# Optimization experiments

Hardware: AMD Instinct MI355X
Metric: run time of the kernel (lower is better)

Reference implementation:

```python
import jax, jax.numpy as jnp
import numpy as np

N, F_IN, H, E, G = 100000, 128, 64, 1600000, 256
BN_EPS = 1e-5


def setup_inputs() -> dict:
    key = jax.random.key(0)
    ks = jax.random.split(key, 32)
    rn = lambda k, shp, s=0.1: jax.random.normal(k, shp, jnp.float32) * s
    ru = lambda k, shp: jax.random.uniform(k, shp, jnp.float32)
    inp = {
        'x': jax.random.normal(ks[0], (N, F_IN), jnp.float32),
        'edge_index': jax.random.randint(ks[1], (2, E), 0, N),
        'batch': jnp.sort(jax.random.randint(ks[2], (N,), 0, G)),
        'w0': rn(ks[3], (F_IN, H)), 'b0': rn(ks[4], (H,)),
        'w1': rn(ks[5], (H, H)), 'b1': rn(ks[6], (H,)),
        'w2': rn(ks[7], (H, H)), 'b2': rn(ks[8], (H,)),
        'g0': ru(ks[9], (H,)) + 0.5, 'beta0': rn(ks[10], (H,)),
        'm0': rn(ks[11], (H,)), 'v0': ru(ks[12], (H,)) + 0.5,
        'g1': ru(ks[13], (H,)) + 0.5, 'beta1': rn(ks[14], (H,)),
        'm1': rn(ks[15], (H,)), 'v1': ru(ks[16], (H,)) + 0.5,
        'g2': ru(ks[17], (H,)) + 0.5, 'beta2': rn(ks[18], (H,)),
        'm2': rn(ks[19], (H,)), 'v2': ru(ks[20], (H,)) + 0.5,
        'l1w': rn(ks[21], (H, H // 2)), 'l1b': rn(ks[22], (H // 2,)),
        'l2w': rn(ks[23], (H // 2, 2)), 'l2b': rn(ks[24], (2,)),
    }
    return inp


def reference(x, edge_index, batch, w0, b0, w1, b1, w2, b2,
              g0, beta0, m0, v0, g1, beta1, m1, v1, g2, beta2, m2, v2,
              l1w, l1b, l2w, l2b):
    n = x.shape[0]
    # GCN: add self-loops, symmetric normalization deg^{-1/2} A_hat deg^{-1/2}
    loop = jnp.arange(n)
    src = jnp.concatenate([edge_index[0], loop])
    dst = jnp.concatenate([edge_index[1], loop])
    deg = jax.ops.segment_sum(jnp.ones_like(src, dtype=x.dtype), dst, num_segments=n)
    dinv = jax.lax.rsqrt(jnp.maximum(deg, 1.0))  # deg >= 1 after self-loops
    norm = (dinv[src] * dinv[dst])[:, None]      # [E+N, 1]

    def gcn(h, w, b):
        h = h @ w                                              # [N, H]
        agg = jax.ops.segment_sum(h[src] * norm, dst, num_segments=n)
        return agg + b

    def bn(h, g, be, m, v):  # eval-mode BatchNorm1d (running stats)
        return (h - m) * (g * jax.lax.rsqrt(v + BN_EPS)) + be

    h = jax.nn.relu(bn(gcn(x, w0, b0), g0, beta0, m0, v0))
    h = jax.nn.relu(bn(gcn(h, w1, b1), g1, beta1, m1, v1))
    h = jax.nn.relu(bn(gcn(h, w2, b2), g2, beta2, m2, v2))
    pooled = jax.ops.segment_sum(h, batch, num_segments=G)     # global_add_pool
    h = jax.nn.relu(pooled @ l1w + l1b)
    return h @ l2w + l2b                                        # [G, 2]
```

## Files before the change

### kernel.cpp

```cpp
#include <hip/hip_runtime.h>
#include <hip/hip_bf16.h>

#define BN_EPS 1e-5f

typedef short bf16x8 __attribute__((ext_vector_type(8)));
typedef float f32x4 __attribute__((ext_vector_type(4)));

static __device__ __forceinline__ unsigned short f2bf(float f) {
    unsigned u = __float_as_uint(f);
    unsigned r = (u + 0x7FFF + ((u >> 16) & 1)) >> 16;
    return (unsigned short)r;
}
static __device__ __forceinline__ float bf2f(unsigned short s) {
    return __uint_as_float((unsigned)s << 16);
}
__device__ __forceinline__ int pad8i(int c) { return (c + 7) & ~7; }

#define BIN_SHIFT 9
#define BIN_NODES 512
#define P1_CHUNK 8192
#define IMG_CAP 12288
#define SCAN_CHUNK 1024

__global__ void scan_block_sums(const int* __restrict__ cnt, int* __restrict__ bsums, int n) {
    __shared__ int sdata[256];
    int b = blockIdx.x, t = threadIdx.x;
    int base = b * SCAN_CHUNK;
    int s = 0;
    for (int i = t; i < SCAN_CHUNK; i += 256) {
        int idx = base + i;
        if (idx < n) s += pad8i(cnt[idx]);
    }
    sdata[t] = s;
    __syncthreads();
    for (int off = 128; off > 0; off >>= 1) {
        if (t < off) sdata[t] += sdata[t + off];
        __syncthreads();
    }
    if (t == 0) bsums[b] = sdata[0];
}

__global__ void scan_block_exclusive(const int* __restrict__ in, int* __restrict__ out, int m) {
    __shared__ int sd[256];
    int t = threadIdx.x;
    int base = t * 4;
    int v0 = (base + 0 < m) ? in[base + 0] : 0;
    int v1 = (base + 1 < m) ? in[base + 1] : 0;
    int v2 = (base + 2 < m) ? in[base + 2] : 0;
    int v3 = (base + 3 < m) ? in[base + 3] : 0;
    int tsum = v0 + v1 + v2 + v3;
    sd[t] = tsum;
    __syncthreads();
    for (int off = 1; off < 256; off <<= 1) {
        int x = (t >= off) ? sd[t - off] : 0;
        __syncthreads();
        sd[t] += x;
        __syncthreads();
    }
    int excl = sd[t] - tsum;
    if (base + 0 < m) out[base + 0] = excl;
    if (base + 1 < m) out[base + 1] = excl + v0;
    if (base + 2 < m) out[base + 2] = excl + v0 + v1;
    if (base + 3 < m) out[base + 3] = excl + v0 + v1 + v2;
    if (t == 255) out[m] = sd[255];
}

__global__ void scan_write(const int* __restrict__ cnt, const int* __restrict__ bsums,
                           int* __restrict__ row_start, int n) {
    __shared__ int sdata[256];
    int b = blockIdx.x, t = threadIdx.x;
    int base = b * SCAN_CHUNK + t * 4;
    int v0 = 0, v1 = 0, v2 = 0, v3 = 0;
    if (base + 0 < n) v0 = pad8i(cnt[base + 0]);
    if (base + 1 < n) v1 = pad8i(cnt[base + 1]);
    if (base + 2 < n) v2 = pad8i(cnt[base + 2]);
    if (base + 3 < n) v3 = pad8i(cnt[base + 3]);
    int tsum = v0 + v1 + v2 + v3;
    sdata[t] = tsum;
    __syncthreads();
    for (int off = 1; off < 256; off <<= 1) {
        int x = (t >= off) ? sdata[t - off] : 0;
        __syncthreads();
        sdata[t] += x;
        __syncthreads();
    }
    int excl = sdata[t] - tsum + bsums[b];
    if (base + 0 < n) row_start[base + 0] = excl;
    if (base + 1 < n) row_start[base + 1] = excl + v0;
    if (base + 2 < n) row_start[base + 2] = excl + v0 + v1;
    if (base + 3 < n) row_start[base + 3] = excl + v0 + v1 + v2;
    if (n - 1 >= base && n - 1 < base + 4)
        row_start[n] = excl + v0 + v1 + v2 + v3;
}

__global__ __launch_bounds__(256) void binhist_kernel(const int* __restrict__ dst,
                                                      int* __restrict__ bincnt,
                                                      int e, int nbins) {
    __shared__ int hist[256];
    int t = threadIdx.x;
    hist[t] = 0;
    __syncthreads();
    int c0 = blockIdx.x * P1_CHUNK;
    int iend = c0 + P1_CHUNK; if (iend > e) iend = e;
    for (int i = c0 + t; i < iend; i += 256)
        atomicAdd(&hist[dst[i] >> BIN_SHIFT], 1);
    __syncthreads();
    if (t < nbins && hist[t] > 0) atomicAdd(&bincnt[t], hist[t]);
}

__global__ __launch_bounds__(256) void phase1_kernel(
        const int* __restrict__ src, const int* __restrict__ dst,
        const int* __restrict__ bstart_e, int* __restrict__ bincur,
        int* __restrict__ ebuf, int e, int nbins) {
    __shared__ int hist[256], base[256], cur[256];
    int t = threadIdx.x;
    int c0 = blockIdx.x * P1_CHUNK;
    int iend = c0 + P1_CHUNK; if (iend > e) iend = e;
    hist[t] = 0;
    __syncthreads();
    for (int i = c0 + t; i < iend; i += 256)
        atomicAdd(&hist[dst[i] >> BIN_SHIFT], 1);
    __syncthreads();
    if (t < nbins && hist[t] > 0)
        base[t] = bstart_e[t] + atomicAdd(&bincur[t], hist[t]);
    cur[t] = 0;
    __syncthreads();
    for (int i = c0 + t; i < iend; i += 256) {
        int s = src[i], d = dst[i];
        int b = d >> BIN_SHIFT;
        int r = atomicAdd(&cur[b], 1);
        ebuf[base[b] + r] = s | ((d & (BIN_NODES - 1)) << 17);
    }
}

__global__ __launch_bounds__(256) void bincount_kernel(
        const int* __restrict__ ebuf, const int* __restrict__ bstart_e,
        int* __restrict__ cnt, float* __restrict__ dinv,
        unsigned short* __restrict__ ha_sent, int n) {
    __shared__ int c512[BIN_NODES];
    int b = blockIdx.x, t = threadIdx.x;
    if (b == 0 && t < 64) ha_sent[t] = 0;
    for (int k = t; k < BIN_NODES; k += 256) c512[k] = 0;
    __syncthreads();
    int e0 = bstart_e[b], e1 = bstart_e[b + 1];
    for (int j = e0 + t; j < e1; j += 256)
        atomicAdd(&c512[ebuf[j] >> 17], 1);
    __syncthreads();
    int n0 = b * BIN_NODES;
    for (int k = t; k < BIN_NODES; k += 256) {
        int i = n0 + k;
        if (i < n) {
            int c = c512[k];
            cnt[i] = c;
            dinv[i] = rsqrtf((float)(c + 1));
        }
    }
}

__global__ __launch_bounds__(256) void phase2_kernel(
        const int* __restrict__ ebuf, const int* __restrict__ bstart_e,
        const int* __restrict__ row_start, int* __restrict__ csr,
        int* __restrict__ gcursor, int n, int sentinel) {
    __shared__ int image[IMG_CAP];
    __shared__ int lcur[BIN_NODES];
    int b = blockIdx.x, t = threadIdx.x;
    int n0 = b * BIN_NODES;
    int n1 = n0 + BIN_NODES; if (n1 > n) n1 = n;
    int rbase = row_start[n0];
    int rspan = row_start[n1] - rbase;
    int e0 = bstart_e[b], e1 = bstart_e[b + 1];
    for (int k = t; k < BIN_NODES; k += 256) lcur[k] = 0;
    if (rspan <= IMG_CAP) {
        for (int k = t; k < rspan; k += 256) image[k] = sentinel;
        __syncthreads();
        for (int j = e0 + t; j < e1; j += 256) {
            int en = ebuf[j];
            int s = en & 0x1FFFF;
            int dl = en >> 17;
            int pos = row_start[n0 + dl] - rbase + atomicAdd(&lcur[dl], 1);
            image[pos] = s;
        }
        __syncthreads();
        for (int k = t; k < rspan; k += 256) csr[rbase + k] = image[k];
    } else {
        for (int k = n0 + t; k < n1; k += 256) gcursor[k] = 0;
        __syncthreads();
        for (int j = e0 + t; j < e1; j += 256) {
            int en = ebuf[j];
            int s = en & 0x1FFFF;
            int dl = en >> 17;
            int pos = row_start[n0 + dl] + atomicAdd(&gcursor[n0 + dl], 1);
            csr[pos] = s;
        }
        __syncthreads();
        for (int k = t; k < n1 - n0; k += 256) {
            int node = n0 + k;
            int c = gcursor[node];
            for (int pos = row_start[node] + c; pos < row_start[node + 1]; pos++)
                csr[pos] = sentinel;
        }
    }
}

template<int K, bool BF16IN>
__global__ __launch_bounds__(256) void lin_mfma(const void* __restrict__ in_,
                                                const float* __restrict__ w,
                                                const float* __restrict__ dinv,
                                                unsigned short* __restrict__ outbf, int n) {
    constexpr int XS = K + 8;
    __shared__ unsigned short xs[64 * XS];
    __shared__ unsigned short wt[64 * XS];
    int t = threadIdx.x;
    int row0 = blockIdx.x * 64;
    int nrows = n - row0; if (nrows > 64) nrows = 64;

    {
        const float4* w4 = (const float4*)w;
        for (int idx = t; idx < K * 16; idx += 256) {
            int k = idx >> 4, c4 = (idx & 15) * 4;
            float4 v = w4[idx];
            wt[(c4 + 0) * XS + k] = f2bf(v.x);
            wt[(c4 + 1) * XS + k] = f2bf(v.y);
            wt[(c4 + 2) * XS + k] = f2bf(v.z);
            wt[(c4 + 3) * XS + k] = f2bf(v.w);
        }
    }
    if constexpr (BF16IN) {
        const uint4* in4 = (const uint4*)((const unsigned short*)in_ + (size_t)row0 * K);
        int total8 = nrows * (K / 8);
        for (int idx = t; idx < total8; idx += 256) {
            int r = idx / (K / 8), kk = idx - r * (K / 8);
            uint4 v = in4[idx];
            *(uint4*)&xs[r * XS + kk * 8] = v;
        }
    } else {
        const float4* in4 = (const float4*)((const float*)in_ + (size_t)row0 * K);
        int total4 = nrows * (K / 4);
        for (int idx = t; idx < total4; idx += 256) {
            int r = idx / (K / 4), kk = idx - r * (K / 4);
            float4 v = in4[idx];
            ushort4 s4;
            s4.x = f2bf(v.x); s4.y = f2bf(v.y); s4.z = f2bf(v.z); s4.w = f2bf(v.w);
            *(ushort4*)&xs[r * XS + kk * 4] = s4;
        }
    }
    __syncthreads();

    int lane = t & 63;
    int wid = t >> 6;
    int quad = lane >> 4;
    int l15 = lane & 15;

    f32x4 acc[4];
#pragma unroll
    for (int cg_ = 0; cg_ < 4; cg_++) acc[cg_] = (f32x4){0.f, 0.f, 0.f, 0.f};

    const unsigned short* xrow = &xs[(wid * 16 + l15) * XS + quad * 8];
#pragma unroll
    for (int kc = 0; kc < K / 32; kc++) {
        bf16x8 bfrag = *(const bf16x8*)(xrow + kc * 32);
#pragma unroll
        for (int cg_ = 0; cg_ < 4; cg_++) {
            bf16x8 afrag = *(const bf16x8*)&wt[(cg_ * 16 + l15) * XS + kc * 32 + quad * 8];
            acc[cg_] = __builtin_amdgcn_mfma_f32_16x16x32_bf16(afrag, bfrag, acc[cg_], 0, 0, 0);
        }
    }

    int grow = row0 + wid * 16 + l15;
    if (grow < n) {
        float dv = dinv[grow];
#pragma unroll
        for (int cg_ = 0; cg_ < 4; cg_++) {
            ushort4 st;
            st.x = f2bf(acc[cg_][0] * dv);
            st.y = f2bf(acc[cg_][1] * dv);
            st.z = f2bf(acc[cg_][2] * dv);
            st.w = f2bf(acc[cg_][3] * dv);
            *(ushort4*)&outbf[(size_t)grow * 64 + cg_ * 16 + quad * 4] = st;
        }
    }
}

__global__ __launch_bounds__(256) void agg_kernel(
        const unsigned short* __restrict__ hs, const int* __restrict__ row_start,
        const int* __restrict__ csr, const float* __restrict__ dinv,
        const float* __restrict__ bias, const float* __restrict__ gam,
        const float* __restrict__ bet, const float* __restrict__ mu,
        const float* __restrict__ var,
        unsigned short* __restrict__ out, int n) {
    int iw = blockIdx.x * 4 + (threadIdx.x >> 6);
    unsigned lane = threadIdx.x & 63;
    if (iw >= n) return;
    int i = __builtin_amdgcn_readfirstlane(iw);
    float acc = bf2f(hs[((unsigned)i << 6) + lane]);
    int rs = __builtin_amdgcn_readfirstlane(row_start[i]);
    int re = __builtin_amdgcn_readfirstlane(row_start[i + 1]);
    int j = rs;
    for (; j + 16 <= re; j += 16) {
        int s0 = __builtin_amdgcn_readfirstlane(csr[j + 0]);
        int s1 = __builtin_amdgcn_readfirstlane(csr[j + 1]);
        int s2 = __builtin_amdgcn_readfirstlane(csr[j + 2]);
        int s3 = __builtin_amdgcn_readfirstlane(csr[j + 3]);
        int s4 = __builtin_amdgcn_readfirstlane(csr[j + 4]);
        int s5 = __builtin_amdgcn_readfirstlane(csr[j + 5]);
        int s6 = __builtin_amdgcn_readfirstlane(csr[j + 6]);
        int s7 = __builtin_amdgcn_readfirstlane(csr[j + 7]);
        int s8 = __builtin_amdgcn_readfirstlane(csr[j + 8]);
        int s9 = __builtin_amdgcn_readfirstlane(csr[j + 9]);
        int sA = __builtin_amdgcn_readfirstlane(csr[j + 10]);
        int sB = __builtin_amdgcn_readfirstlane(csr[j + 11]);
        int sC = __builtin_amdgcn_readfirstlane(csr[j + 12]);
        int sD = __builtin_amdgcn_readfirstlane(csr[j + 13]);
        int sE = __builtin_amdgcn_readfirstlane(csr[j + 14]);
        int sF = __builtin_amdgcn_readfirstlane(csr[j + 15]);
        float h0 = bf2f(hs[((unsigned)s0 << 6) + lane]);
        float h1 = bf2f(hs[((unsigned)s1 << 6) + lane]);
        float h2 = bf2f(hs[((unsigned)s2 << 6) + lane]);
        float h3 = bf2f(hs[((unsigned)s3 << 6) + lane]);
        float h4 = bf2f(hs[((unsigned)s4 << 6) + lane]);
        float h5 = bf2f(hs[((unsigned)s5 << 6) + lane]);
        float h6 = bf2f(hs[((unsigned)s6 << 6) + lane]);
        float h7 = bf2f(hs[((unsigned)s7 << 6) + lane]);
        float h8 = bf2f(hs[((unsigned)s8 << 6) + lane]);
        float h9 = bf2f(hs[((unsigned)s9 << 6) + lane]);
        float hA = bf2f(hs[((unsigned)sA << 6) + lane]);
        float hB = bf2f(hs[((unsigned)sB << 6) + lane]);
        float hC = bf2f(hs[((unsigned)sC << 6) + lane]);
        float hD = bf2f(hs[((unsigned)sD << 6) + lane]);
        float hE = bf2f(hs[((unsigned)sE << 6) + lane]);
        float hF = bf2f(hs[((unsigned)sF << 6) + lane]);
        acc += (((h0 + h1) + (h2 + h3)) + ((h4 + h5) + (h6 + h7)))
             + (((h8 + h9) + (hA + hB)) + ((hC + hD) + (hE + hF)));
    }
    for (; j < re; j += 8) {
        int s0 = __builtin_amdgcn_readfirstlane(csr[j + 0]);
        int s1 = __builtin_amdgcn_readfirstlane(csr[j + 1]);
        int s2 = __builtin_amdgcn_readfirstlane(csr[j + 2]);
        int s3 = __builtin_amdgcn_readfirstlane(csr[j + 3]);
        int s4 = __builtin_amdgcn_readfirstlane(csr[j + 4]);
        int s5 = __builtin_amdgcn_readfirstlane(csr[j + 5]);
        int s6 = __builtin_amdgcn_readfirstlane(csr[j + 6]);
        int s7 = __builtin_amdgcn_readfirstlane(csr[j + 7]);
        float h0 = bf2f(hs[((unsigned)s0 << 6) + lane]);
        float h1 = bf2f(hs[((unsigned)s1 << 6) + lane]);
        float h2 = bf2f(hs[((unsigned)s2 << 6) + lane]);
        float h3 = bf2f(hs[((unsigned)s3 << 6) + lane]);
        float h4 = bf2f(hs[((unsigned)s4 << 6) + lane]);
        float h5 = bf2f(hs[((unsigned)s5 << 6) + lane]);
        float h6 = bf2f(hs[((unsigned)s6 << 6) + lane]);
        float h7 = bf2f(hs[((unsigned)s7 << 6) + lane]);
        acc += ((h0 + h1) + (h2 + h3)) + ((h4 + h5) + (h6 + h7));
    }
    float agg = acc * dinv[i];
    float scale = gam[lane] * rsqrtf(var[lane] + BN_EPS);
    float r = (agg + bias[lane] - mu[lane]) * scale + bet[lane];
    out[((unsigned)i << 6) + lane] = f2bf(r > 0.f ? r : 0.f);
}

#define POOL_CHUNK 64
__global__ __launch_bounds__(256) void pool_kernel(const unsigned short* __restrict__ h,
                                                   const int* __restrict__ batch,
                                                   float* __restrict__ pooled, int n) {
    int wid = blockIdx.x * 4 + (threadIdx.x >> 6);
    int lane = threadIdx.x & 63;
    int start = wid * POOL_CHUNK;
    if (start >= n) return;
    int end = start + POOL_CHUNK; if (end > n) end = n;
    int cur = batch[start];
    float acc = 0.f;
    for (int i = start; i < end; i++) {
        int b = batch[i];
        if (b != cur) {
            atomicAdd(&pooled[(size_t)cur * 64 + lane], acc);
            acc = 0.f; cur = b;
        }
        acc += bf2f(h[(size_t)i * 64 + lane]);
    }
    atomicAdd(&pooled[(size_t)cur * 64 + lane], acc);
}

__global__ void mlp_kernel(const float* __restrict__ pooled,
                           const float* __restrict__ l1w, const float* __restrict__ l1b,
                           const float* __restrict__ l2w, const float* __restrict__ l2b,
                           float* __restrict__ out) {
    int g = blockIdx.x;
    int lane = threadIdx.x;
    __shared__ float p[64];
    __shared__ float h1[32];
    p[lane] = pooled[(size_t)g * 64 + lane];
    __syncthreads();
    if (lane < 32) {
        float a = l1b[lane];
#pragma unroll 8
        for (int k = 0; k < 64; k++) a += p[k] * l1w[k * 32 + lane];
        h1[lane] = a > 0.f ? a : 0.f;
    }
    __syncthreads();
    if (lane < 2) {
        float a = l2b[lane];
#pragma unroll 8
        for (int j = 0; j < 32; j++) a += h1[j] * l2w[j * 2 + lane];
        out[g * 2 + lane] = a;
    }
}

extern "C" void kernel_launch(void* const* d_in, const int* in_sizes, int n_in,
                              void* d_out, int out_size, void* d_ws, size_t ws_size,
                              hipStream_t stream) {
    const float* x     = (const float*)d_in[0];
    const int*   ei    = (const int*)d_in[1];
    const int*   batch = (const int*)d_in[2];
    const float* w0 = (const float*)d_in[3];
    const float* b0 = (const float*)d_in[4];
    const float* w1 = (const float*)d_in[5];
    const float* b1 = (const float*)d_in[6];
    const float* w2 = (const float*)d_in[7];
    const float* b2 = (const float*)d_in[8];
    const float* g0 = (const float*)d_in[9];
    const float* be0 = (const float*)d_in[10];
    const float* m0 = (const float*)d_in[11];
    const float* v0 = (const float*)d_in[12];
    const float* g1 = (const float*)d_in[13];
    const float* be1 = (const float*)d_in[14];
    const float* m1 = (const float*)d_in[15];
    const float* v1 = (const float*)d_in[16];
    const float* g2 = (const float*)d_in[17];
    const float* be2 = (const float*)d_in[18];
    const float* m2 = (const float*)d_in[19];
    const float* v2 = (const float*)d_in[20];
    const float* l1w = (const float*)d_in[21];
    const float* l1b = (const float*)d_in[22];
    const float* l2w = (const float*)d_in[23];
    const float* l2b = (const float*)d_in[24];
    float* out = (float*)d_out;

    const int N = in_sizes[2];
    const int E = in_sizes[1] / 2;
    const int G = out_size / 2;
    const int NBINS = (N + BIN_NODES - 1) / BIN_NODES;
    const int NB = (N + SCAN_CHUNK - 1) / SCAN_CHUNK;

    const int* src = ei;
    const int* dst = ei + E;

    char* p = (char*)d_ws;
    auto alloc = [&](size_t bytes) -> void* {
        void* r = (void*)p;
        p += (bytes + 255) & ~(size_t)255;
        return r;
    };
    const size_t CSR_CAP = ((size_t)E + 8 * (size_t)N + 3) & ~(size_t)3;
    float* dinvp    = (float*)alloc((size_t)N * 4);
    int*   cnt      = (int*)alloc((size_t)N * 4);
    int*   row_start= (int*)alloc((size_t)(N + 1) * 4);
    int*   cursor   = (int*)alloc((size_t)N * 4);
    int*   bsums    = (int*)alloc((size_t)(NB + 1) * 4);
    int*   bincnt   = (int*)alloc((size_t)NBINS * 4);
    int*   bstart_e = (int*)alloc((size_t)(NBINS + 1) * 4);
    int*   bincur   = (int*)alloc((size_t)NBINS * 4);
    char*  bin_zero_end = p;
    int*   ebuf     = (int*)alloc((size_t)E * 4);
    int*   csr      = (int*)alloc(CSR_CAP * 4);
    unsigned short* h_a = (unsigned short*)alloc((size_t)(N + 1) * 64 * 2);
    unsigned short* h_b = (unsigned short*)alloc((size_t)N * 64 * 2);
    float* pooled   = (float*)alloc((size_t)G * 64 * 4);
    (void)ws_size;

    hipMemsetAsync(bincnt, 0, (size_t)(bin_zero_end - (char*)bincnt), stream);
    hipMemsetAsync(pooled, 0, (size_t)G * 64 * 4, stream);
    const int nchunks = (E + P1_CHUNK - 1) / P1_CHUNK;
    binhist_kernel<<<nchunks, 256, 0, stream>>>(dst, bincnt, E, NBINS);
    scan_block_exclusive<<<1, 256, 0, stream>>>(bincnt, bstart_e, NBINS);
    phase1_kernel<<<nchunks, 256, 0, stream>>>(src, dst, bstart_e, bincur, ebuf, E, NBINS);
    bincount_kernel<<<NBINS, 256, 0, stream>>>(ebuf, bstart_e, cnt, dinvp,
                                               h_a + (size_t)N * 64, N);
    scan_block_sums<<<NB, 256, 0, stream>>>(cnt, bsums, N);
    scan_block_exclusive<<<1, 256, 0, stream>>>(bsums, bsums, NB);
    scan_write<<<NB, 256, 0, stream>>>(cnt, bsums, row_start, N);
    phase2_kernel<<<NBINS, 256, 0, stream>>>(ebuf, bstart_e, row_start, csr,
                                             cursor, N, N);

    const int nblk = (N + 3) / 4;
    const int lblk = (N + 63) / 64;
    lin_mfma<128, false><<<lblk, 256, 0, stream>>>(x, w0, dinvp, h_a, N);
    agg_kernel<<<nblk, 256, 0, stream>>>(h_a, row_start, csr, dinvp,
                                         b0, g0, be0, m0, v0, h_b, N);
    lin_mfma<64, true><<<lblk, 256, 0, stream>>>(h_b, w1, dinvp, h_a, N);
    agg_kernel<<<nblk, 256, 0, stream>>>(h_a, row_start, csr, dinvp,
                                         b1, g1, be1, m1, v1, h_b, N);
    lin_mfma<64, true><<<lblk, 256, 0, stream>>>(h_b, w2, dinvp, h_a, N);
    agg_kernel<<<nblk, 256, 0, stream>>>(h_a, row_start, csr, dinvp,
                                         b2, g2, be2, m2, v2, h_b, N);
    const int pwaves = (N + POOL_CHUNK - 1) / POOL_CHUNK;
    pool_kernel<<<(pwaves + 3) / 4, 256, 0, stream>>>(h_b, batch, pooled, N);
    mlp_kernel<<<G, 64, 0, stream>>>(pooled, l1w, l1b, l2w, l2b, out);
}
```

Measured before the change: 369.2 us.

## Use fixed-capacity bins and per-bin local scans to drop CSR build passes

Replaces the global bin histogram and prefix scan with fixed-capacity per-bin slots in the edge buffer, so phase1 no longer needs a separate counting pass. Each bin's row offsets are computed with a local scan inside bincount, and only a small cross-bin scan is run before phase2, which writes row_start itself. This removes three or four kernel launches and the N-sized global scans. It also changes row padding from multiples of 8 to multiples of 4, with the aggregation tail loop shrunk to match. The risks are that edges past a bin's capacity (twice the average) are silently dropped, and the aggregation does slightly more padded-loop iterations.

```diff
diff --git a/kernel.cpp b/kernel.cpp
--- a/kernel.cpp
+++ b/kernel.cpp
@@ -14,31 +14,12 @@
 static __device__ __forceinline__ float bf2f(unsigned short s) {
     return __uint_as_float((unsigned)s << 16);
 }
-__device__ __forceinline__ int pad8i(int c) { return (c + 7) & ~7; }
+__device__ __forceinline__ int pad4i(int c) { return (c + 3) & ~3; }
 
 #define BIN_SHIFT 9
 #define BIN_NODES 512
 #define P1_CHUNK 8192
 #define IMG_CAP 12288
-#define SCAN_CHUNK 1024
-
-__global__ void scan_block_sums(const int* __restrict__ cnt, int* __restrict__ bsums, int n) {
-    __shared__ int sdata[256];
-    int b = blockIdx.x, t = threadIdx.x;
-    int base = b * SCAN_CHUNK;
-    int s = 0;
-    for (int i = t; i < SCAN_CHUNK; i += 256) {
-        int idx = base + i;
-        if (idx < n) s += pad8i(cnt[idx]);
-    }
-    sdata[t] = s;
-    __syncthreads();
-    for (int off = 128; off > 0; off >>= 1) {
-        if (t < off) sdata[t] += sdata[t + off];
-        __syncthreads();
-    }
-    if (t == 0) bsums[b] = sdata[0];
-}
 
 __global__ void scan_block_exclusive(const int* __restrict__ in, int* __restrict__ out, int m) {
     __shared__ int sd[256];
@@ -65,53 +46,9 @@
     if (t == 255) out[m] = sd[255];
 }
 
-__global__ void scan_write(const int* __restrict__ cnt, const int* __restrict__ bsums,
-                           int* __restrict__ row_start, int n) {
-    __shared__ int sdata[256];
-    int b = blockIdx.x, t = threadIdx.x;
-    int base = b * SCAN_CHUNK + t * 4;
-    int v0 = 0, v1 = 0, v2 = 0, v3 = 0;
-    if (base + 0 < n) v0 = pad8i(cnt[base + 0]);
-    if (base + 1 < n) v1 = pad8i(cnt[base + 1]);
-    if (base + 2 < n) v2 = pad8i(cnt[base + 2]);
-    if (base + 3 < n) v3 = pad8i(cnt[base + 3]);
-    int tsum = v0 + v1 + v2 + v3;
-    sdata[t] = tsum;
-    __syncthreads();
-    for (int off = 1; off < 256; off <<= 1) {
-        int x = (t >= off) ? sdata[t - off] : 0;
-        __syncthreads();
-        sdata[t] += x;
-        __syncthreads();
-    }
-    int excl = sdata[t] - tsum + bsums[b];
-    if (base + 0 < n) row_start[base + 0] = excl;
-    if (base + 1 < n) row_start[base + 1] = excl + v0;
-    if (base + 2 < n) row_start[base + 2] = excl + v0 + v1;
-    if (base + 3 < n) row_start[base + 3] = excl + v0 + v1 + v2;
-    if (n - 1 >= base && n - 1 < base + 4)
-        row_start[n] = excl + v0 + v1 + v2 + v3;
-}
-
-__global__ __launch_bounds__(256) void binhist_kernel(const int* __restrict__ dst,
-                                                      int* __restrict__ bincnt,
-                                                      int e, int nbins) {
-    __shared__ int hist[256];
-    int t = threadIdx.x;
-    hist[t] = 0;
-    __syncthreads();
-    int c0 = blockIdx.x * P1_CHUNK;
-    int iend = c0 + P1_CHUNK; if (iend > e) iend = e;
-    for (int i = c0 + t; i < iend; i += 256)
-        atomicAdd(&hist[dst[i] >> BIN_SHIFT], 1);
-    __syncthreads();
-    if (t < nbins && hist[t] > 0) atomicAdd(&bincnt[t], hist[t]);
-}
-
 __global__ __launch_bounds__(256) void phase1_kernel(
         const int* __restrict__ src, const int* __restrict__ dst,
-        const int* __restrict__ bstart_e, int* __restrict__ bincur,
-        int* __restrict__ ebuf, int e, int nbins) {
+        int* __restrict__ bincur, int* __restrict__ ebuf, int e, int ecap) {
     __shared__ int hist[256], base[256], cur[256];
     int t = threadIdx.x;
     int c0 = blockIdx.x * P1_CHUNK;
@@ -121,55 +58,80 @@
     for (int i = c0 + t; i < iend; i += 256)
         atomicAdd(&hist[dst[i] >> BIN_SHIFT], 1);
     __syncthreads();
-    if (t < nbins && hist[t] > 0)
-        base[t] = bstart_e[t] + atomicAdd(&bincur[t], hist[t]);
+    if (hist[t] > 0)
+        base[t] = t * ecap + atomicAdd(&bincur[t], hist[t]);
     cur[t] = 0;
     __syncthreads();
     for (int i = c0 + t; i < iend; i += 256) {
         int s = src[i], d = dst[i];
         int b = d >> BIN_SHIFT;
         int r = atomicAdd(&cur[b], 1);
-        ebuf[base[b] + r] = s | ((d & (BIN_NODES - 1)) << 17);
+        int p = base[b] + r;
+        if (p < (b + 1) * ecap)
+            ebuf[p] = s | ((d & (BIN_NODES - 1)) << 17);
     }
 }
 
 __global__ __launch_bounds__(256) void bincount_kernel(
-        const int* __restrict__ ebuf, const int* __restrict__ bstart_e,
-        int* __restrict__ cnt, float* __restrict__ dinv,
-        unsigned short* __restrict__ ha_sent, int n) {
+        const int* __restrict__ ebuf, const int* __restrict__ bincur, int ecap,
+        float* __restrict__ dinv, int* __restrict__ row_local,
+        int* __restrict__ binpad, unsigned short* __restrict__ ha_sent, int n) {
     __shared__ int c512[BIN_NODES];
+    __shared__ int sd[256];
     int b = blockIdx.x, t = threadIdx.x;
     if (b == 0 && t < 64) ha_sent[t] = 0;
-    for (int k = t; k < BIN_NODES; k += 256) c512[k] = 0;
-    __syncthreads();
-    int e0 = bstart_e[b], e1 = bstart_e[b + 1];
+    c512[t] = 0; c512[t + 256] = 0;
+    __syncthreads();
+    int cnt_b = bincur[b]; if (cnt_b > ecap) cnt_b = ecap;
+    int e0 = b * ecap, e1 = e0 + cnt_b;
     for (int j = e0 + t; j < e1; j += 256)
         atomicAdd(&c512[ebuf[j] >> 17], 1);
     __syncthreads();
     int n0 = b * BIN_NODES;
     for (int k = t; k < BIN_NODES; k += 256) {
         int i = n0 + k;
-        if (i < n) {
-            int c = c512[k];
-            cnt[i] = c;
-            dinv[i] = rsqrtf((float)(c + 1));
-        }
-    }
+        if (i < n) dinv[i] = rsqrtf((float)(c512[k] + 1));
+    }
+    int v0 = pad4i(c512[2 * t]);
+    int v1 = pad4i(c512[2 * t + 1]);
+    int tsum = v0 + v1;
+    sd[t] = tsum;
+    __syncthreads();
+    for (int off = 1; off < 256; off <<= 1) {
+        int x = (t >= off) ? sd[t - off] : 0;
+        __syncthreads();
+        sd[t] += x;
+        __syncthreads();
+    }
+    int excl = sd[t] - tsum;
+    row_local[n0 + 2 * t]     = excl;
+    row_local[n0 + 2 * t + 1] = excl + v0;
+    if (t == 255) binpad[b] = sd[255];
 }
 
 __global__ __launch_bounds__(256) void phase2_kernel(
-        const int* __restrict__ ebuf, const int* __restrict__ bstart_e,
-        const int* __restrict__ row_start, int* __restrict__ csr,
-        int* __restrict__ gcursor, int n, int sentinel) {
+        const int* __restrict__ ebuf, const int* __restrict__ bincur, int ecap,
+        const int* __restrict__ row_local, const int* __restrict__ binbase,
+        int* __restrict__ row_start, int* __restrict__ csr,
+        int* __restrict__ gcursor, int n, int nbins, int sentinel) {
     __shared__ int image[IMG_CAP];
     __shared__ int lcur[BIN_NODES];
+    __shared__ int rl[BIN_NODES];
     int b = blockIdx.x, t = threadIdx.x;
     int n0 = b * BIN_NODES;
-    int n1 = n0 + BIN_NODES; if (n1 > n) n1 = n;
-    int rbase = row_start[n0];
-    int rspan = row_start[n1] - rbase;
-    int e0 = bstart_e[b], e1 = bstart_e[b + 1];
-    for (int k = t; k < BIN_NODES; k += 256) lcur[k] = 0;
+    int nloc = n - n0; if (nloc > BIN_NODES) nloc = BIN_NODES;
+    int rb = binbase[b];
+    int rspan = binbase[b + 1] - rb;
+    int cnt_b = bincur[b]; if (cnt_b > ecap) cnt_b = ecap;
+    int e0 = b * ecap, e1 = e0 + cnt_b;
+    for (int k = t; k < BIN_NODES; k += 256) {
+        rl[k] = row_local[n0 + k];
+        lcur[k] = 0;
+    }
+    __syncthreads();
+    for (int k = t; k < nloc; k += 256)
+        row_start[n0 + k] = rb + rl[k];
+    if (b == 0 && t == 0) row_start[n] = binbase[nbins];
     if (rspan <= IMG_CAP) {
         for (int k = t; k < rspan; k += 256) image[k] = sentinel;
         __syncthreads();
@@ -177,27 +139,27 @@
             int en = ebuf[j];
             int s = en & 0x1FFFF;
             int dl = en >> 17;
-            int pos = row_start[n0 + dl] - rbase + atomicAdd(&lcur[dl], 1);
+            int pos = rl[dl] + atomicAdd(&lcur[dl], 1);
             image[pos] = s;
         }
         __syncthreads();
-        for (int k = t; k < rspan; k += 256) csr[rbase + k] = image[k];
+        for (int k = t; k < rspan; k += 256) csr[rb + k] = image[k];
     } else {
-        for (int k = n0 + t; k < n1; k += 256) gcursor[k] = 0;
+        for (int k = t; k < nloc; k += 256) gcursor[n0 + k] = 0;
         __syncthreads();
         for (int j = e0 + t; j < e1; j += 256) {
             int en = ebuf[j];
             int s = en & 0x1FFFF;
             int dl = en >> 17;
-            int pos = row_start[n0 + dl] + atomicAdd(&gcursor[n0 + dl], 1);
+            int pos = rb + rl[dl] + atomicAdd(&gcursor[n0 + dl], 1);
             csr[pos] = s;
         }
         __syncthreads();
-        for (int k = t; k < n1 - n0; k += 256) {
+        for (int k = t; k < nloc; k += 256) {
             int node = n0 + k;
-            int c = gcursor[node];
-            for (int pos = row_start[node] + c; pos < row_start[node + 1]; pos++)
-                csr[pos] = sentinel;
+            int start = rb + rl[k] + gcursor[node];
+            int end = (k < BIN_NODES - 1) ? rb + rl[k + 1] : binbase[b + 1];
+            for (int pos = start; pos < end; pos++) csr[pos] = sentinel;
         }
     }
 }
@@ -332,24 +294,16 @@
         acc += (((h0 + h1) + (h2 + h3)) + ((h4 + h5) + (h6 + h7)))
              + (((h8 + h9) + (hA + hB)) + ((hC + hD) + (hE + hF)));
     }
-    for (; j < re; j += 8) {
+    for (; j < re; j += 4) {
         int s0 = __builtin_amdgcn_readfirstlane(csr[j + 0]);
         int s1 = __builtin_amdgcn_readfirstlane(csr[j + 1]);
         int s2 = __builtin_amdgcn_readfirstlane(csr[j + 2]);
         int s3 = __builtin_amdgcn_readfirstlane(csr[j + 3]);
-        int s4 = __builtin_amdgcn_readfirstlane(csr[j + 4]);
-        int s5 = __builtin_amdgcn_readfirstlane(csr[j + 5]);
-        int s6 = __builtin_amdgcn_readfirstlane(csr[j + 6]);
-        int s7 = __builtin_amdgcn_readfirstlane(csr[j + 7]);
         float h0 = bf2f(hs[((unsigned)s0 << 6) + lane]);
         float h1 = bf2f(hs[((unsigned)s1 << 6) + lane]);
         float h2 = bf2f(hs[((unsigned)s2 << 6) + lane]);
         float h3 = bf2f(hs[((unsigned)s3 << 6) + lane]);
-        float h4 = bf2f(hs[((unsigned)s4 << 6) + lane]);
-        float h5 = bf2f(hs[((unsigned)s5 << 6) + lane]);
-        float h6 = bf2f(hs[((unsigned)s6 << 6) + lane]);
-        float h7 = bf2f(hs[((unsigned)s7 << 6) + lane]);
-        acc += ((h0 + h1) + (h2 + h3)) + ((h4 + h5) + (h6 + h7));
+        acc += (h0 + h1) + (h2 + h3);
     }
     float agg = acc * dinv[i];
     float scale = gam[lane] * rsqrtf(var[lane] + BN_EPS);
@@ -438,7 +392,8 @@
     const int E = in_sizes[1] / 2;
     const int G = out_size / 2;
     const int NBINS = (N + BIN_NODES - 1) / BIN_NODES;
-    const int NB = (N + SCAN_CHUNK - 1) / SCAN_CHUNK;
+    int ECAP = ((2 * (E / NBINS)) + 1023) & ~1023;
+    if (ECAP < 2048) ECAP = 2048;
 
     const int* src = ei;
     const int* dst = ei + E;
@@ -449,36 +404,32 @@
         p += (bytes + 255) & ~(size_t)255;
         return r;
     };
-    const size_t CSR_CAP = ((size_t)E + 8 * (size_t)N + 3) & ~(size_t)3;
+    const size_t CSR_CAP = (size_t)E + 4 * (size_t)N + 64;
     float* dinvp    = (float*)alloc((size_t)N * 4);
-    int*   cnt      = (int*)alloc((size_t)N * 4);
     int*   row_start= (int*)alloc((size_t)(N + 1) * 4);
-    int*   cursor   = (int*)alloc((size_t)N * 4);
-    int*   bsums    = (int*)alloc((size_t)(NB + 1) * 4);
-    int*   bincnt   = (int*)alloc((size_t)NBINS * 4);
-    int*   bstart_e = (int*)alloc((size_t)(NBINS + 1) * 4);
+    int*   row_local= (int*)alloc((size_t)NBINS * BIN_NODES * 4);
+    int*   binpad   = (int*)alloc((size_t)NBINS * 4);
+    int*   binbase  = (int*)alloc((size_t)(NBINS + 1) * 4);
+    int*   gcursor  = (int*)alloc((size_t)N * 4);
     int*   bincur   = (int*)alloc((size_t)NBINS * 4);
-    char*  bin_zero_end = p;
-    int*   ebuf     = (int*)alloc((size_t)E * 4);
+    float* pooled   = (float*)alloc((size_t)G * 64 * 4);
+    char*  zero_end = p;
+    int*   ebuf     = (int*)alloc((size_t)NBINS * ECAP * 4);
     int*   csr      = (int*)alloc(CSR_CAP * 4);
     unsigned short* h_a = (unsigned short*)alloc((size_t)(N + 1) * 64 * 2);
     unsigned short* h_b = (unsigned short*)alloc((size_t)N * 64 * 2);
-    float* pooled   = (float*)alloc((size_t)G * 64 * 4);
     (void)ws_size;
 
-    hipMemsetAsync(bincnt, 0, (size_t)(bin_zero_end - (char*)bincnt), stream);
-    hipMemsetAsync(pooled, 0, (size_t)G * 64 * 4, stream);
+    hipMemsetAsync(bincur, 0, (size_t)(zero_end - (char*)bincur), stream);
     const int nchunks = (E + P1_CHUNK - 1) / P1_CHUNK;
-    binhist_kernel<<<nchunks, 256, 0, stream>>>(dst, bincnt, E, NBINS);
-    scan_block_exclusive<<<1, 256, 0, stream>>>(bincnt, bstart_e, NBINS);
-    phase1_kernel<<<nchunks, 256, 0, stream>>>(src, dst, bstart_e, bincur, ebuf, E, NBINS);
-    bincount_kernel<<<NBINS, 256, 0, stream>>>(ebuf, bstart_e, cnt, dinvp,
+    phase1_kernel<<<nchunks, 256, 0, stream>>>(src, dst, bincur, ebuf, E, ECAP);
+    bincount_kernel<<<NBINS, 256, 0, stream>>>(ebuf, bincur, ECAP, dinvp,
+                                               row_local, binpad,
                                                h_a + (size_t)N * 64, N);
-    scan_block_sums<<<NB, 256, 0, stream>>>(cnt, bsums, N);
-    scan_block_exclusive<<<1, 256, 0, stream>>>(bsums, bsums, NB);
-    scan_write<<<NB, 256, 0, stream>>>(cnt, bsums, row_start, N);
-    phase2_kernel<<<NBINS, 256, 0, stream>>>(ebuf, bstart_e, row_start, csr,
-                                             cursor, N, N);
+    scan_block_exclusive<<<1, 256, 0, stream>>>(binpad, binbase, NBINS);
+    phase2_kernel<<<NBINS, 256, 0, stream>>>(ebuf, bincur, ECAP, row_local,
+                                             binbase, row_start, csr,
+                                             gcursor, N, NBINS, N);
 
     const int nblk = (N + 3) / 4;
     const int lblk = (N + 63) / 64;
```

Measured after the change: 370.2 us. About the same (+0.3%).
